# Kernel optimization log

Hardware: AMD Instinct MI355X
Metric: run time of the kernel (lower is better)

## Reference

```python
import jax, jax.numpy as jnp
import numpy as np

N = 50000      # nodes
E = 800000     # edges
FEAT = 128     # node_feat_size
HID = 128      # hidden_channels
LAT = 64       # latent_size
G = 256        # number of graphs in the batch


def _glorot_like(key, fan_in, shape):
    s = 1.0 / np.sqrt(fan_in)
    return jax.random.uniform(key, shape, jnp.float32, -s, s)


def setup_inputs() -> dict:
    key = jax.random.key(0)
    ks = jax.random.split(key, 13)
    x = jax.random.normal(ks[0], (N, FEAT), jnp.float32)
    edge_index = jax.random.randint(ks[1], (2, E), 0, N, dtype=jnp.int64)
    batch = jnp.sort(jax.random.randint(ks[2], (N,), 0, G, dtype=jnp.int64))
    return {
        "x": x,
        "edge_index": edge_index,
        "batch": batch,
        # GCNConv1: FEAT -> HID
        "W1": _glorot_like(ks[3], FEAT, (FEAT, HID)), "b1": jnp.zeros((HID,), jnp.float32),
        # GCNConv2: HID -> HID
        "W2": _glorot_like(ks[4], HID, (HID, HID)), "b2": jnp.zeros((HID,), jnp.float32),
        # fc: HID -> LAT
        "fcW": _glorot_like(ks[5], HID, (HID, LAT)), "fcb": _glorot_like(ks[6], HID, (LAT,)),
        # decoder: LAT -> HID
        "decW": _glorot_like(ks[7], LAT, (LAT, HID)), "decb": _glorot_like(ks[8], LAT, (HID,)),
        # GCNConv3: HID -> FEAT
        "W3": _glorot_like(ks[9], HID, (HID, FEAT)), "b3": jnp.zeros((FEAT,), jnp.float32),
    }


def reference(x, edge_index, batch, W1, b1, W2, b2, fcW, fcb, decW, decb, W3, b3):
    # --- GCN normalization with self-loops (computed once, shared by all convs) ---
    loop = jnp.arange(N, dtype=edge_index.dtype)
    row = jnp.concatenate([edge_index[0], loop])   # source nodes [E+N]
    col = jnp.concatenate([edge_index[1], loop])   # target nodes [E+N]
    deg = jax.ops.segment_sum(jnp.ones(row.shape, x.dtype), col, num_segments=N)
    dinv = jnp.where(deg > 0, jax.lax.rsqrt(deg), jnp.zeros_like(deg))
    norm = dinv[row] * dinv[col]                   # [E+N]

    def gcn(h, W, b):
        h = h @ W                                   # [N, out] transform first (PyG order)
        msg = h[row] * norm[:, None]                # gather + scale, [E+N, out]
        out = jax.ops.segment_sum(msg, col, num_segments=N)  # scatter-add
        return out + b

    # --- encode ---
    h = jax.nn.relu(gcn(x, W1, b1))
    h = jax.nn.relu(gcn(h, W2, b2))
    pooled = jax.ops.segment_sum(h, batch, num_segments=G)   # global_add_pool [G, HID]
    latent = jax.nn.relu(pooled @ fcW + fcb)                 # [G, LAT]

    # --- decode ---
    z = jax.nn.relu(latent @ decW + decb)                    # [G, HID]
    z = z[batch]                                             # broadcast back to nodes [N, HID]
    recon = gcn(z, W3, b3)                                   # [N, FEAT]
    return recon, latent
```

## Files before the change

### kernel.cpp

```cpp
#include <hip/hip_runtime.h>
#include <hip/hip_fp16.h>

static constexpr int NN   = 50000;
static constexpr int EE   = 800000;
static constexpr int GG   = 256;
static constexpr int PCH  = 16;
static constexpr int BK   = 128;
static constexpr int NB   = (NN + BK - 1) / BK;
static constexpr int CAP  = 4096;
static constexpr int CH   = 2048;
static constexpr int ABLK = (EE + CH - 1) / CH;

typedef _Float16 f16;
typedef f16  f16x8 __attribute__((ext_vector_type(8)));
typedef float f32x4 __attribute__((ext_vector_type(4)));

__device__ __forceinline__ int lowerb(const int* __restrict__ b, int n, int v) {
    int lo = 0, hi = n;
    while (lo < hi) { int m = (lo + hi) >> 1; if (b[m] < v) lo = m + 1; else hi = m; }
    return lo;
}

__global__ void init_k(int* __restrict__ bcur)
{
    int b = blockIdx.x * 256 + threadIdx.x;
    if (b < NB) bcur[b] = b * CAP;
}

__global__ __launch_bounds__(512) void binA_k(const int* __restrict__ ei,
                                              int* __restrict__ bcur,
                                              int2* __restrict__ eraw)
{
    __shared__ int2  stage[CH];
    __shared__ short sbid[CH];
    __shared__ int   hist[NB], loff[NB], gbase[NB], lcur[NB];
    __shared__ int   sc[512];

    int tid = threadIdx.x;
    int e0 = blockIdx.x * CH;
    int n = EE - e0; if (n > CH) n = CH;

    for (int b = tid; b < NB; b += 512) hist[b] = 0;
    __syncthreads();

    int2 r[CH / 512];
    #pragma unroll
    for (int k = 0; k < CH / 512; k++) {
        int s = k * 512 + tid;
        if (s < n) {
            int src = ei[e0 + s];
            int dst = ei[EE + e0 + s];
            r[k] = make_int2(src, dst);
            atomicAdd(&hist[dst >> 7], 1);
        }
    }
    __syncthreads();
    int v = (tid < NB) ? hist[tid] : 0;
    sc[tid] = v;
    __syncthreads();
    #pragma unroll
    for (int off = 1; off < 512; off <<= 1) {
        int add = (tid >= off) ? sc[tid - off] : 0;
        __syncthreads();
        sc[tid] += add;
        __syncthreads();
    }
    if (tid < NB) { int ex = sc[tid] - v; loff[tid] = ex; lcur[tid] = ex; }
    __syncthreads();
    for (int b = tid; b < NB; b += 512)
        gbase[b] = atomicAdd(&bcur[b], hist[b]);
    __syncthreads();
    #pragma unroll
    for (int k = 0; k < CH / 512; k++) {
        int s = k * 512 + tid;
        if (s < n) {
            int b = r[k].y >> 7;
            int slot = atomicAdd(&lcur[b], 1);
            stage[slot] = r[k];
            sbid[slot]  = (short)b;
        }
    }
    __syncthreads();
    for (int s = tid; s < n; s += 512) {
        int b = sbid[s];
        eraw[(size_t)gbase[b] + (s - loff[b])] = stage[s];
    }
}

__global__ __launch_bounds__(512) void scanb2_k(const int* __restrict__ bcur,
                                                int* __restrict__ bbase,
                                                int* __restrict__ rowptr)
{
    __shared__ int s[512];
    int t = threadIdx.x;
    int v = (t < NB) ? (bcur[t] - t * CAP) : 0;
    s[t] = v;
    __syncthreads();
    #pragma unroll
    for (int off = 1; off < 512; off <<= 1) {
        int add = (t >= off) ? s[t - off] : 0;
        __syncthreads();
        s[t] += add;
        __syncthreads();
    }
    if (t < NB) bbase[t] = s[t] - v;
    if (t == 0) rowptr[NN] = EE;
}

__global__ __launch_bounds__(512) void binB_k(const int2* __restrict__ eraw,
                                              const int* __restrict__ bcur,
                                              const int* __restrict__ bbase,
                                              int* __restrict__ rowptr,
                                              int* __restrict__ ebuf)
{
    __shared__ int hist[BK], excl[BK], cur[BK];
    int b = blockIdx.x, tid = threadIdx.x;
    int t0 = b << 7;
    int lim = NN - t0; if (lim > BK) lim = BK;
    int tot  = bcur[b] - b * CAP;
    int base = bbase[b];
    const int2* er = eraw + (size_t)b * CAP;

    if (tid < BK) hist[tid] = 0;
    __syncthreads();
    for (int s = tid; s < tot; s += 512) atomicAdd(&hist[er[s].y & 127], 1);
    __syncthreads();
    if (tid < BK) excl[tid] = hist[tid];
    __syncthreads();
    #pragma unroll
    for (int off = 1; off < BK; off <<= 1) {
        int add = (tid >= off && tid < BK) ? excl[tid - off] : 0;
        __syncthreads();
        if (tid < BK) excl[tid] += add;
        __syncthreads();
    }
    if (tid < BK) {
        int ex = excl[tid] - hist[tid];
        cur[tid] = base + ex;
        if (tid < lim) rowptr[t0 + tid] = base + ex;
    }
    __syncthreads();
    for (int s = tid; s < tot; s += 512) {
        int2 rec = er[s];
        int p = atomicAdd(&cur[rec.y & 127], 1);
        ebuf[p] = rec.x;
    }
}

__global__ void dinv_k(const int* __restrict__ rowptr, float* __restrict__ dinv)
{
    int i = blockIdx.x * 256 + threadIdx.x;
    if (i < NN) dinv[i] = rsqrtf((float)(rowptr[i + 1] - rowptr[i] + 1));
}

__global__ void pbb_k(const int* __restrict__ ebuf, const int* __restrict__ batch,
                      const float* __restrict__ dinv, int2* __restrict__ ebuf2)
{
    int e = blockIdx.x * 256 + threadIdx.x;
    if (e < EE) {
        int src = ebuf[e];
        ebuf2[e] = make_int2(batch[src], __float_as_int(dinv[src]));
    }
}

__global__ __launch_bounds__(256) void wprep_k(const float* __restrict__ W,
                                               f16x8* __restrict__ whi_f,
                                               f16x8* __restrict__ wlo_f)
{
    int tid = blockIdx.x * 256 + threadIdx.x;
    int m  = tid & 15;
    int kq = (tid >> 4) & 3;
    int ks = (tid >> 6) & 3;
    int nt = tid >> 8;
    int n  = nt * 16 + m;
    int k0 = ks * 32 + kq * 8;
    f16x8 h8, l8;
    #pragma unroll
    for (int u = 0; u < 8; u++) {
        float x = W[(size_t)(k0 + u) * 128 + n];
        f16 h = (f16)x;
        h8[u] = h;
        l8[u] = (f16)(x - (float)h);
    }
    whi_f[tid] = h8;
    wlo_f[tid] = l8;
}

__global__ __launch_bounds__(256) void gemm_mfma2_k(const float* __restrict__ in,
                                                    const f16x8* __restrict__ whi_f,
                                                    const f16x8* __restrict__ wlo_f,
                                                    const float* __restrict__ dinv,
                                                    __half* __restrict__ out,
                                                    int rows)
{
    int tid  = threadIdx.x;
    int lane = tid & 63;
    int wv   = tid >> 6;
    int rB   = blockIdx.x * 64 + wv * 16;
    int m    = lane & 15;
    int kq   = lane >> 4;
    int r    = rB + m;
    int rr   = (r < rows) ? r : (rows - 1);

    f16x8 ahi[4], alo[4];
    const float* rp = in + (size_t)rr * 128 + kq * 8;
    #pragma unroll
    for (int ks = 0; ks < 4; ks++) {
        float4 p0 = *(const float4*)(rp + ks * 32);
        float4 p1 = *(const float4*)(rp + ks * 32 + 4);
        float xs[8] = {p0.x, p0.y, p0.z, p0.w, p1.x, p1.y, p1.z, p1.w};
        #pragma unroll
        for (int u = 0; u < 8; u++) {
            f16 h = (f16)xs[u];
            ahi[ks][u] = h;
            alo[ks][u] = (f16)(xs[u] - (float)h);
        }
    }

    f32x4 acc[8];
    #pragma unroll
    for (int n = 0; n < 8; n++) acc[n] = (f32x4){0.f, 0.f, 0.f, 0.f};

    #pragma unroll
    for (int nt = 0; nt < 8; nt++) {
        #pragma unroll
        for (int ks = 0; ks < 4; ks++) {
            int idx = ((nt * 4 + ks) * 4 + kq) * 16 + m;
            f16x8 bh = whi_f[idx];
            f16x8 bl = wlo_f[idx];
            acc[nt] = __builtin_amdgcn_mfma_f32_16x16x32_f16(ahi[ks], bh, acc[nt], 0, 0, 0);
            acc[nt] = __builtin_amdgcn_mfma_f32_16x16x32_f16(alo[ks], bh, acc[nt], 0, 0, 0);
            acc[nt] = __builtin_amdgcn_mfma_f32_16x16x32_f16(ahi[ks], bl, acc[nt], 0, 0, 0);
        }
    }

    int   orow[4];
    float dv[4];
    #pragma unroll
    for (int j = 0; j < 4; j++) {
        int gr = rB + kq * 4 + j;
        orow[j] = gr;
        dv[j]   = (gr < rows) ? dinv[gr] : 0.f;
    }
    #pragma unroll
    for (int nt = 0; nt < 8; nt++) {
        int c = nt * 16 + m;
        #pragma unroll
        for (int j = 0; j < 4; j++) {
            if (orow[j] < rows)
                out[(size_t)orow[j] * 128 + c] = __float2half(acc[nt][j] * dv[j]);
        }
    }
}

__device__ __forceinline__ float4 gat4h(const __half* __restrict__ t, int s, int q)
{
    uint2 v = *(const uint2*)(t + ((size_t)s << 7) + q * 4);
    __half2 a = __builtin_bit_cast(__half2, v.x);
    __half2 b = __builtin_bit_cast(__half2, v.y);
    float2 fa = __half22float2(a), fb = __half22float2(b);
    return make_float4(fa.x, fa.y, fb.x, fb.y);
}

__global__ __launch_bounds__(64) void aggh_k(const __half* __restrict__ t,
                                             const int* __restrict__ rowptr,
                                             const int* __restrict__ ebuf,
                                             const float* __restrict__ dinv,
                                             const float* __restrict__ bias,
                                             float* __restrict__ out,
                                             int relu)
{
    int i    = blockIdx.x;
    int lane = threadIdx.x;
    int half = lane >> 5;
    int q    = lane & 31;

    float a0 = 0.f, a1 = 0.f, a2 = 0.f, a3 = 0.f;
    if (half == 0) {
        float4 v = gat4h(t, i, q);
        a0 = v.x; a1 = v.y; a2 = v.z; a3 = v.w;
    }

    int e0 = __builtin_amdgcn_readfirstlane(rowptr[i]);
    int e1 = __builtin_amdgcn_readfirstlane(rowptr[i + 1]);
    int deg = e1 - e0;
    int full = deg & ~7;
    int ee = e0 + full;
    for (int e = e0 + half * 4; e < ee; e += 8) {
        int s0 = ebuf[e],     s1 = ebuf[e + 1];
        int s2 = ebuf[e + 2], s3 = ebuf[e + 3];
        float4 w0 = gat4h(t, s0, q);
        float4 w1 = gat4h(t, s1, q);
        float4 w2 = gat4h(t, s2, q);
        float4 w3 = gat4h(t, s3, q);
        a0 += w0.x + w1.x + w2.x + w3.x;
        a1 += w0.y + w1.y + w2.y + w3.y;
        a2 += w0.z + w1.z + w2.z + w3.z;
        a3 += w0.w + w1.w + w2.w + w3.w;
    }
    for (int e = ee + half; e < e1; e += 2) {
        float4 w = gat4h(t, ebuf[e], q);
        a0 += w.x; a1 += w.y; a2 += w.z; a3 += w.w;
    }
    a0 += __shfl_xor(a0, 32);
    a1 += __shfl_xor(a1, 32);
    a2 += __shfl_xor(a2, 32);
    a3 += __shfl_xor(a3, 32);

    if (half == 0) {
        float di = dinv[i];
        float4 b = *(const float4*)(bias + q * 4);
        float4 o;
        o.x = di * a0 + b.x;
        o.y = di * a1 + b.y;
        o.z = di * a2 + b.z;
        o.w = di * a3 + b.w;
        if (relu) {
            o.x = fmaxf(o.x, 0.f); o.y = fmaxf(o.y, 0.f);
            o.z = fmaxf(o.z, 0.f); o.w = fmaxf(o.w, 0.f);
        }
        *(float4*)(out + (size_t)i * 128 + q * 4) = o;
    }
}

__global__ __launch_bounds__(64) void agg_out_k(const float* __restrict__ zz,
                                                const int* __restrict__ batch,
                                                const int* __restrict__ rowptr,
                                                const int2* __restrict__ ebuf2,
                                                const float* __restrict__ dinv,
                                                const float* __restrict__ bias,
                                                float* __restrict__ out)
{
    int i    = blockIdx.x;
    int lane = threadIdx.x;
    int half = lane >> 5;
    int q    = lane & 31;
    float di = dinv[i];

    float a0 = 0.f, a1 = 0.f, a2 = 0.f, a3 = 0.f;
    if (half == 0) {
        float4 v = *(const float4*)(zz + ((size_t)batch[i] << 7) + q * 4);
        a0 = di * v.x; a1 = di * v.y; a2 = di * v.z; a3 = di * v.w;
    }

    int e0 = rowptr[i], e1 = rowptr[i + 1];
    int deg = e1 - e0;
    int full = deg & ~7;
    int ee = e0 + full;
    for (int e = e0 + half * 4; e < ee; e += 8) {
        int2 r0 = ebuf2[e],     r1 = ebuf2[e + 1];
        int2 r2 = ebuf2[e + 2], r3 = ebuf2[e + 3];
        float4 w0 = *(const float4*)(zz + ((size_t)r0.x << 7) + q * 4);
        float4 w1 = *(const float4*)(zz + ((size_t)r1.x << 7) + q * 4);
        float4 w2 = *(const float4*)(zz + ((size_t)r2.x << 7) + q * 4);
        float4 w3 = *(const float4*)(zz + ((size_t)r3.x << 7) + q * 4);
        float n0 = __int_as_float(r0.y), n1 = __int_as_float(r1.y);
        float n2 = __int_as_float(r2.y), n3 = __int_as_float(r3.y);
        a0 += n0 * w0.x + n1 * w1.x + n2 * w2.x + n3 * w3.x;
        a1 += n0 * w0.y + n1 * w1.y + n2 * w2.y + n3 * w3.y;
        a2 += n0 * w0.z + n1 * w1.z + n2 * w2.z + n3 * w3.z;
        a3 += n0 * w0.w + n1 * w1.w + n2 * w2.w + n3 * w3.w;
    }
    for (int e = ee + half; e < e1; e += 2) {
        int2 r = ebuf2[e];
        float nm = __int_as_float(r.y);
        float4 w = *(const float4*)(zz + ((size_t)r.x << 7) + q * 4);
        a0 += nm * w.x; a1 += nm * w.y; a2 += nm * w.z; a3 += nm * w.w;
    }
    a0 += __shfl_xor(a0, 32);
    a1 += __shfl_xor(a1, 32);
    a2 += __shfl_xor(a2, 32);
    a3 += __shfl_xor(a3, 32);

    if (half == 0) {
        float4 b = *(const float4*)(bias + q * 4);
        float4 o;
        o.x = di * a0 + b.x;
        o.y = di * a1 + b.y;
        o.z = di * a2 + b.z;
        o.w = di * a3 + b.w;
        *(float4*)(out + (size_t)i * 128 + q * 4) = o;
    }
}

__global__ __launch_bounds__(128) void pool2_k(const float* __restrict__ h2,
                                               const int* __restrict__ batch,
                                               float* __restrict__ pooled)
{
    int g = blockIdx.x;
    int c = blockIdx.y;
    int f = threadIdx.x;
    int bs = lowerb(batch, NN, g);
    int be = lowerb(batch, NN, g + 1);
    int len = be - bs;
    int cs = bs + (int)(((long long)len * c) / PCH);
    int ce = bs + (int)(((long long)len * (c + 1)) / PCH);
    float a = 0.f;
    for (int i = cs; i < ce; i++) a += h2[(size_t)i * 128 + f];
    if (ce > cs) atomicAdd(&pooled[(size_t)g * 128 + f], a);
}

__global__ __launch_bounds__(64) void fc_k(const float* __restrict__ pooled,
                                           const float* __restrict__ fcW,
                                           const float* __restrict__ fcb,
                                           float* __restrict__ latentf,
                                           float* __restrict__ lat_out)
{
    int g = blockIdx.x, l = threadIdx.x;
    const float* p = pooled + (size_t)g * 128;
    float a = fcb[l];
    #pragma unroll 8
    for (int k = 0; k < 128; k++) a = fmaf(p[k], fcW[(size_t)k * 64 + l], a);
    a = fmaxf(a, 0.f);
    latentf[(size_t)g * 64 + l] = a;
    lat_out[(size_t)g * 64 + l] = a;
}

__global__ __launch_bounds__(128) void dec_k(const float* __restrict__ latentf,
                                             const float* __restrict__ decW,
                                             const float* __restrict__ decb,
                                             const float* __restrict__ W3,
                                             float* __restrict__ zz)
{
    __shared__ float zs[128];
    int g = blockIdx.x, c = threadIdx.x;
    const float* lat = latentf + (size_t)g * 64;
    {
        float a = decb[c];
        #pragma unroll 8
        for (int k = 0; k < 64; k++) a = fmaf(lat[k], decW[(size_t)k * 128 + c], a);
        zs[c] = fmaxf(a, 0.f);
    }
    __syncthreads();
    float o = 0.f;
    #pragma unroll 8
    for (int k = 0; k < 128; k++) o = fmaf(zs[k], W3[(size_t)k * 128 + c], o);
    zz[(size_t)g * 128 + c] = o;
}

extern "C" void kernel_launch(void* const* d_in, const int* in_sizes, int n_in,
                              void* d_out, int out_size, void* d_ws, size_t ws_size,
                              hipStream_t stream)
{
    const float* x     = (const float*)d_in[0];
    const int*   ei    = (const int*)d_in[1];
    const int*   batch = (const int*)d_in[2];
    const float* W1  = (const float*)d_in[3];
    const float* b1  = (const float*)d_in[4];
    const float* W2  = (const float*)d_in[5];
    const float* b2  = (const float*)d_in[6];
    const float* fcW = (const float*)d_in[7];
    const float* fcb = (const float*)d_in[8];
    const float* decW= (const float*)d_in[9];
    const float* decb= (const float*)d_in[10];
    const float* W3  = (const float*)d_in[11];
    const float* b3  = (const float*)d_in[12];

    char* ws = (char*)d_ws;
    size_t off = 0;
    auto alloc = [&](size_t bytes) -> char* {
        char* p = ws + off;
        off = (off + bytes + 255) & ~(size_t)255;
        return p;
    };
    float* dinv     = (float*)alloc((size_t)NN * 4);
    int*   rowptr   = (int*)alloc((size_t)(NN + 1) * 4);
    int*   bcur     = (int*)alloc((size_t)NB * 4);
    int*   bbase    = (int*)alloc((size_t)NB * 4);
    int*   ebuf     = (int*)alloc((size_t)EE * 4);
    float* pooled   = (float*)alloc((size_t)GG * 128 * 4);
    float* latentf  = (float*)alloc((size_t)GG * 64 * 4);
    float* zz       = (float*)alloc((size_t)GG * 128 * 4);
    f16x8* whi1     = (f16x8*)alloc(2048 * 16);
    f16x8* wlo1     = (f16x8*)alloc(2048 * 16);
    f16x8* whi2     = (f16x8*)alloc(2048 * 16);
    f16x8* wlo2     = (f16x8*)alloc(2048 * 16);
    __half* A       = (__half*)alloc((size_t)NN * 128 * 2);
    float* B        = (float*)alloc((size_t)NN * 128 * 4);
    int2*  eraw     = (int2*)B;
    int2*  ebuf2    = (int2*)A;

    float* recon_out = (float*)d_out;
    float* lat_out   = (float*)d_out + (size_t)NN * 128;

    hipMemsetAsync(pooled, 0, (size_t)GG * 128 * 4, stream);
    init_k<<<(NB + 255) / 256, 256, 0, stream>>>(bcur);
    binA_k<<<ABLK, 512, 0, stream>>>(ei, bcur, eraw);
    scanb2_k<<<1, 512, 0, stream>>>(bcur, bbase, rowptr);
    binB_k<<<NB, 512, 0, stream>>>(eraw, bcur, bbase, rowptr, ebuf);
    dinv_k<<<(NN + 255) / 256, 256, 0, stream>>>(rowptr, dinv);
    wprep_k<<<8, 256, 0, stream>>>(W1, whi1, wlo1);
    wprep_k<<<8, 256, 0, stream>>>(W2, whi2, wlo2);

    int gblk = (NN + 63) / 64;
    gemm_mfma2_k<<<gblk, 256, 0, stream>>>(x, whi1, wlo1, dinv, A, NN);
    aggh_k<<<NN, 64, 0, stream>>>(A, rowptr, ebuf, dinv, b1, B, 1);
    gemm_mfma2_k<<<gblk, 256, 0, stream>>>(B, whi2, wlo2, dinv, A, NN);
    aggh_k<<<NN, 64, 0, stream>>>(A, rowptr, ebuf, dinv, b2, B, 1);
    pbb_k<<<(EE + 255) / 256, 256, 0, stream>>>(ebuf, batch, dinv, ebuf2);
    pool2_k<<<dim3(GG, PCH), 128, 0, stream>>>(B, batch, pooled);
    fc_k<<<GG, 64, 0, stream>>>(pooled, fcW, fcb, latentf, lat_out);
    dec_k<<<GG, 128, 0, stream>>>(latentf, decW, decb, W3, zz);
    agg_out_k<<<NN, 64, 0, stream>>>(zz, batch, rowptr, ebuf2, dinv,
                                     b3, recon_out);
}
```

Measured before the change: 302.0 us.

## Fuse small kernels, stage weights in LDS, and prefetch edge indices via shuffles

Folds the degree-inverse computation into the binning kernel and merges the two weight-prep launches and the fc/decoder kernels, cutting launch count. The GEMM now stages the high-half weights in shared memory. The aggregation kernel loads up to 64 neighbour indices in one coalesced read and distributes them by lane shuffles, with 8-wide unrolled gathers. ebuf2 gets its own buffer so pbb_k can run early, at the cost of more workspace and extra shared-memory use in the GEMM.

```diff
diff --git a/kernel.cpp b/kernel.cpp
--- a/kernel.cpp
+++ b/kernel.cpp
@@ -111,6 +111,7 @@
                                               const int* __restrict__ bcur,
                                               const int* __restrict__ bbase,
                                               int* __restrict__ rowptr,
+                                              float* __restrict__ dinv,
                                               int* __restrict__ ebuf)
 {
     __shared__ int hist[BK], excl[BK], cur[BK];
@@ -137,7 +138,10 @@
     if (tid < BK) {
         int ex = excl[tid] - hist[tid];
         cur[tid] = base + ex;
-        if (tid < lim) rowptr[t0 + tid] = base + ex;
+        if (tid < lim) {
+            rowptr[t0 + tid] = base + ex;
+            dinv[t0 + tid]   = rsqrtf((float)(hist[tid] + 1));
+        }
     }
     __syncthreads();
     for (int s = tid; s < tot; s += 512) {
@@ -147,12 +151,6 @@
     }
 }
 
-__global__ void dinv_k(const int* __restrict__ rowptr, float* __restrict__ dinv)
-{
-    int i = blockIdx.x * 256 + threadIdx.x;
-    if (i < NN) dinv[i] = rsqrtf((float)(rowptr[i + 1] - rowptr[i] + 1));
-}
-
 __global__ void pbb_k(const int* __restrict__ ebuf, const int* __restrict__ batch,
                       const float* __restrict__ dinv, int2* __restrict__ ebuf2)
 {
@@ -163,11 +161,16 @@
     }
 }
 
-__global__ __launch_bounds__(256) void wprep_k(const float* __restrict__ W,
-                                               f16x8* __restrict__ whi_f,
-                                               f16x8* __restrict__ wlo_f)
-{
-    int tid = blockIdx.x * 256 + threadIdx.x;
+__global__ __launch_bounds__(256) void wprep2_k(const float* __restrict__ W1,
+                                                const float* __restrict__ W2,
+                                                f16x8* __restrict__ whi1, f16x8* __restrict__ wlo1,
+                                                f16x8* __restrict__ whi2, f16x8* __restrict__ wlo2)
+{
+    int blk = blockIdx.x;
+    const float* W = (blk < 8) ? W1 : W2;
+    f16x8* wh = (blk < 8) ? whi1 : whi2;
+    f16x8* wl = (blk < 8) ? wlo1 : wlo2;
+    int tid = (blk & 7) * 256 + threadIdx.x;
     int m  = tid & 15;
     int kq = (tid >> 4) & 3;
     int ks = (tid >> 6) & 3;
@@ -182,18 +185,23 @@
         h8[u] = h;
         l8[u] = (f16)(x - (float)h);
     }
-    whi_f[tid] = h8;
-    wlo_f[tid] = l8;
-}
-
-__global__ __launch_bounds__(256) void gemm_mfma2_k(const float* __restrict__ in,
+    wh[tid] = h8;
+    wl[tid] = l8;
+}
+
+__global__ __launch_bounds__(256) void gemm_mfma3_k(const float* __restrict__ in,
                                                     const f16x8* __restrict__ whi_f,
                                                     const f16x8* __restrict__ wlo_f,
                                                     const float* __restrict__ dinv,
                                                     __half* __restrict__ out,
                                                     int rows)
 {
+    __shared__ __align__(16) f16x8 sh[2048];
     int tid  = threadIdx.x;
+    #pragma unroll
+    for (int u = 0; u < 8; u++) sh[u * 256 + tid] = whi_f[u * 256 + tid];
+    __syncthreads();
+
     int lane = tid & 63;
     int wv   = tid >> 6;
     int rB   = blockIdx.x * 64 + wv * 16;
@@ -226,7 +234,7 @@
         #pragma unroll
         for (int ks = 0; ks < 4; ks++) {
             int idx = ((nt * 4 + ks) * 4 + kq) * 16 + m;
-            f16x8 bh = whi_f[idx];
+            f16x8 bh = sh[idx];
             f16x8 bl = wlo_f[idx];
             acc[nt] = __builtin_amdgcn_mfma_f32_16x16x32_f16(ahi[ks], bh, acc[nt], 0, 0, 0);
             acc[nt] = __builtin_amdgcn_mfma_f32_16x16x32_f16(alo[ks], bh, acc[nt], 0, 0, 0);
@@ -275,20 +283,42 @@
     int half = lane >> 5;
     int q    = lane & 31;
 
+    int e0 = __builtin_amdgcn_readfirstlane(rowptr[i]);
+    int e1 = __builtin_amdgcn_readfirstlane(rowptr[i + 1]);
+    int deg = e1 - e0;
+    int idxsafe = (deg > 0) ? (e0 + min(lane, deg - 1)) : 0;
+    int myidx = ebuf[idxsafe];
+
     float a0 = 0.f, a1 = 0.f, a2 = 0.f, a3 = 0.f;
     if (half == 0) {
         float4 v = gat4h(t, i, q);
         a0 = v.x; a1 = v.y; a2 = v.z; a3 = v.w;
     }
 
-    int e0 = __builtin_amdgcn_readfirstlane(rowptr[i]);
-    int e1 = __builtin_amdgcn_readfirstlane(rowptr[i + 1]);
-    int deg = e1 - e0;
-    int full = deg & ~7;
-    int ee = e0 + full;
-    for (int e = e0 + half * 4; e < ee; e += 8) {
-        int s0 = ebuf[e],     s1 = ebuf[e + 1];
-        int s2 = ebuf[e + 2], s3 = ebuf[e + 3];
+    int v   = min(deg, 64);
+    int c16 = v & ~15;
+    for (int j = half * 8; j < c16; j += 16) {
+        int s0 = __shfl(myidx, j + 0), s1 = __shfl(myidx, j + 1);
+        int s2 = __shfl(myidx, j + 2), s3 = __shfl(myidx, j + 3);
+        int s4 = __shfl(myidx, j + 4), s5 = __shfl(myidx, j + 5);
+        int s6 = __shfl(myidx, j + 6), s7 = __shfl(myidx, j + 7);
+        float4 w0 = gat4h(t, s0, q);
+        float4 w1 = gat4h(t, s1, q);
+        float4 w2 = gat4h(t, s2, q);
+        float4 w3 = gat4h(t, s3, q);
+        float4 w4 = gat4h(t, s4, q);
+        float4 w5 = gat4h(t, s5, q);
+        float4 w6 = gat4h(t, s6, q);
+        float4 w7 = gat4h(t, s7, q);
+        a0 += w0.x + w1.x + w2.x + w3.x + w4.x + w5.x + w6.x + w7.x;
+        a1 += w0.y + w1.y + w2.y + w3.y + w4.y + w5.y + w6.y + w7.y;
+        a2 += w0.z + w1.z + w2.z + w3.z + w4.z + w5.z + w6.z + w7.z;
+        a3 += w0.w + w1.w + w2.w + w3.w + w4.w + w5.w + w6.w + w7.w;
+    }
+    if (v - c16 >= 8) {
+        int j = c16 + half * 4;
+        int s0 = __shfl(myidx, j + 0), s1 = __shfl(myidx, j + 1);
+        int s2 = __shfl(myidx, j + 2), s3 = __shfl(myidx, j + 3);
         float4 w0 = gat4h(t, s0, q);
         float4 w1 = gat4h(t, s1, q);
         float4 w2 = gat4h(t, s2, q);
@@ -298,10 +328,17 @@
         a2 += w0.z + w1.z + w2.z + w3.z;
         a3 += w0.w + w1.w + w2.w + w3.w;
     }
-    for (int e = ee + half; e < e1; e += 2) {
+    int done = c16 + ((v - c16) & 8);
+    for (int j = done + half; j < v; j += 2) {
+        int s = __shfl(myidx, j);
+        float4 w = gat4h(t, s, q);
+        a0 += w.x; a1 += w.y; a2 += w.z; a3 += w.w;
+    }
+    for (int e = e0 + 64 + half; e < e1; e += 2) {
         float4 w = gat4h(t, ebuf[e], q);
         a0 += w.x; a1 += w.y; a2 += w.z; a3 += w.w;
     }
+
     a0 += __shfl_xor(a0, 32);
     a1 += __shfl_xor(a1, 32);
     a2 += __shfl_xor(a2, 32);
@@ -400,31 +437,28 @@
     if (ce > cs) atomicAdd(&pooled[(size_t)g * 128 + f], a);
 }
 
-__global__ __launch_bounds__(64) void fc_k(const float* __restrict__ pooled,
-                                           const float* __restrict__ fcW,
-                                           const float* __restrict__ fcb,
-                                           float* __restrict__ latentf,
-                                           float* __restrict__ lat_out)
-{
-    int g = blockIdx.x, l = threadIdx.x;
-    const float* p = pooled + (size_t)g * 128;
-    float a = fcb[l];
-    #pragma unroll 8
-    for (int k = 0; k < 128; k++) a = fmaf(p[k], fcW[(size_t)k * 64 + l], a);
-    a = fmaxf(a, 0.f);
-    latentf[(size_t)g * 64 + l] = a;
-    lat_out[(size_t)g * 64 + l] = a;
-}
-
-__global__ __launch_bounds__(128) void dec_k(const float* __restrict__ latentf,
-                                             const float* __restrict__ decW,
-                                             const float* __restrict__ decb,
-                                             const float* __restrict__ W3,
-                                             float* __restrict__ zz)
-{
+__global__ __launch_bounds__(128) void fcdec_k(const float* __restrict__ pooled,
+                                               const float* __restrict__ fcW,
+                                               const float* __restrict__ fcb,
+                                               const float* __restrict__ decW,
+                                               const float* __restrict__ decb,
+                                               const float* __restrict__ W3,
+                                               float* __restrict__ lat_out,
+                                               float* __restrict__ zz)
+{
+    __shared__ float lat[64];
     __shared__ float zs[128];
     int g = blockIdx.x, c = threadIdx.x;
-    const float* lat = latentf + (size_t)g * 64;
+    if (c < 64) {
+        const float* p = pooled + (size_t)g * 128;
+        float a = fcb[c];
+        #pragma unroll 8
+        for (int k = 0; k < 128; k++) a = fmaf(p[k], fcW[(size_t)k * 64 + c], a);
+        a = fmaxf(a, 0.f);
+        lat[c] = a;
+        lat_out[(size_t)g * 64 + c] = a;
+    }
+    __syncthreads();
     {
         float a = decb[c];
         #pragma unroll 8
@@ -468,8 +502,8 @@
     int*   bcur     = (int*)alloc((size_t)NB * 4);
     int*   bbase    = (int*)alloc((size_t)NB * 4);
     int*   ebuf     = (int*)alloc((size_t)EE * 4);
+    int2*  ebuf2    = (int2*)alloc((size_t)EE * 8);
     float* pooled   = (float*)alloc((size_t)GG * 128 * 4);
-    float* latentf  = (float*)alloc((size_t)GG * 64 * 4);
     float* zz       = (float*)alloc((size_t)GG * 128 * 4);
     f16x8* whi1     = (f16x8*)alloc(2048 * 16);
     f16x8* wlo1     = (f16x8*)alloc(2048 * 16);
@@ -478,7 +512,6 @@
     __half* A       = (__half*)alloc((size_t)NN * 128 * 2);
     float* B        = (float*)alloc((size_t)NN * 128 * 4);
     int2*  eraw     = (int2*)B;
-    int2*  ebuf2    = (int2*)A;
 
     float* recon_out = (float*)d_out;
     float* lat_out   = (float*)d_out + (size_t)NN * 128;
@@ -487,20 +520,17 @@
     init_k<<<(NB + 255) / 256, 256, 0, stream>>>(bcur);
     binA_k<<<ABLK, 512, 0, stream>>>(ei, bcur, eraw);
     scanb2_k<<<1, 512, 0, stream>>>(bcur, bbase, rowptr);
-    binB_k<<<NB, 512, 0, stream>>>(eraw, bcur, bbase, rowptr, ebuf);
-    dinv_k<<<(NN + 255) / 256, 256, 0, stream>>>(rowptr, dinv);
-    wprep_k<<<8, 256, 0, stream>>>(W1, whi1, wlo1);
-    wprep_k<<<8, 256, 0, stream>>>(W2, whi2, wlo2);
+    binB_k<<<NB, 512, 0, stream>>>(eraw, bcur, bbase, rowptr, dinv, ebuf);
+    wprep2_k<<<16, 256, 0, stream>>>(W1, W2, whi1, wlo1, whi2, wlo2);
+    pbb_k<<<(EE + 255) / 256, 256, 0, stream>>>(ebuf, batch, dinv, ebuf2);
 
     int gblk = (NN + 63) / 64;
-    gemm_mfma2_k<<<gblk, 256, 0, stream>>>(x, whi1, wlo1, dinv, A, NN);
+    gemm_mfma3_k<<<gblk, 256, 0, stream>>>(x, whi1, wlo1, dinv, A, NN);
     aggh_k<<<NN, 64, 0, stream>>>(A, rowptr, ebuf, dinv, b1, B, 1);
-    gemm_mfma2_k<<<gblk, 256, 0, stream>>>(B, whi2, wlo2, dinv, A, NN);
+    gemm_mfma3_k<<<gblk, 256, 0, stream>>>(B, whi2, wlo2, dinv, A, NN);
     aggh_k<<<NN, 64, 0, stream>>>(A, rowptr, ebuf, dinv, b2, B, 1);
-    pbb_k<<<(EE + 255) / 256, 256, 0, stream>>>(ebuf, batch, dinv, ebuf2);
     pool2_k<<<dim3(GG, PCH), 128, 0, stream>>>(B, batch, pooled);
-    fc_k<<<GG, 64, 0, stream>>>(pooled, fcW, fcb, latentf, lat_out);
-    dec_k<<<GG, 128, 0, stream>>>(latentf, decW, decb, W3, zz);
+    fcdec_k<<<GG, 128, 0, stream>>>(pooled, fcW, fcb, decW, decb, W3, lat_out, zz);
     agg_out_k<<<NN, 64, 0, stream>>>(zz, batch, rowptr, ebuf2, dinv,
                                      b3, recon_out);
 }
```

Measured after the change: 288.8 us. -4.4%, faster.
